# Kernel optimization log

Measured on AMD Instinct MI355X. Metric: run time of the kernel, lower is better.

Reference implementation:

```python
import jax, jax.numpy as jnp
import numpy as np

N = 100000   # nodes
E = 3200000  # edges (avg degree 32)
F_IN = 128   # nfeat
H = 128      # nhid
C = 40       # nclass
L = 3        # nlayers (GRU steps in GatedGraphConv)
BN_EPS = 1e-5


def _uniform(k, shape, scale):
    return jax.random.uniform(k, shape, jnp.float32, -scale, scale)


def setup_inputs() -> dict:
    key = jax.random.key(0)
    ks = jax.random.split(key, 12)
    h = jax.random.normal(ks[0], (N, F_IN), jnp.float32)
    edge_index = jax.random.randint(ks[1], (2, E), 0, N, dtype=jnp.int64)
    edge_weight = jax.random.uniform(ks[2], (E,), jnp.float32)
    s_h = 1.0 / np.sqrt(H)
    s_f = 1.0 / np.sqrt(F_IN)
    emb_W = _uniform(ks[3], (F_IN, H), s_f)
    emb_b = _uniform(ks[4], (H,), s_f)
    conv_weight = _uniform(ks[5], (L, H, H), s_h)      # PyG GatedGraphConv.weight
    gru_Wih = _uniform(ks[6], (3 * H, H), s_h)         # torch GRUCell weight_ih
    gru_Whh = _uniform(ks[7], (3 * H, H), s_h)
    gru_bih = _uniform(ks[8], (3 * H,), s_h)
    gru_bhh = _uniform(ks[9], (3 * H,), s_h)
    bn_gamma = jnp.ones((H,), jnp.float32)
    bn_beta = jnp.zeros((H,), jnp.float32)
    mlp_W = _uniform(ks[10], (H, C), s_h)
    mlp_b = _uniform(ks[11], (C,), s_h)
    return {"h": h, "edge_index": edge_index, "edge_weight": edge_weight,
            "emb_W": emb_W, "emb_b": emb_b, "conv_weight": conv_weight,
            "gru_Wih": gru_Wih, "gru_Whh": gru_Whh, "gru_bih": gru_bih,
            "gru_bhh": gru_bhh, "bn_gamma": bn_gamma, "bn_beta": bn_beta,
            "mlp_W": mlp_W, "mlp_b": mlp_b}


def reference(h, edge_index, edge_weight, emb_W, emb_b, conv_weight,
              gru_Wih, gru_Whh, gru_bih, gru_bhh, bn_gamma, bn_beta,
              mlp_W, mlp_b):
    src, dst = edge_index[0], edge_index[1]
    x = h @ emb_W + emb_b                      # [N, H] embedding_h
    h_in = x                                   # residual tap (before conv)
    for i in range(L):                         # GatedGraphConv GRU steps
        m = x @ conv_weight[i]                 # [N, H]
        msg = edge_weight[:, None] * m[src]    # [E, H] gather + weight
        agg = jax.ops.segment_sum(msg, dst, num_segments=N)  # scatter-add
        gi = agg @ gru_Wih.T + gru_bih         # [N, 3H]
        gh = x @ gru_Whh.T + gru_bhh
        i_r, i_z, i_n = jnp.split(gi, 3, axis=1)
        h_r, h_z, h_n = jnp.split(gh, 3, axis=1)
        r = jax.nn.sigmoid(i_r + h_r)
        z = jax.nn.sigmoid(i_z + h_z)
        n = jnp.tanh(i_n + r * h_n)
        x = (1.0 - z) * n + z * x              # GRUCell update
    mean = jnp.mean(x, axis=0)                 # BatchNorm1d (training stats)
    var = jnp.var(x, axis=0)
    x = (x - mean) / jnp.sqrt(var + BN_EPS) * bn_gamma + bn_beta
    x = h_in + x                               # residual; dropout p=0 is identity
    return x @ mlp_W + mlp_b                   # [N, C]
```

## Files before the change

### kernel.cpp

```cpp
#include <hip/hip_runtime.h>
#include <math.h>

#define N_NODES 100000
#define N_EDGES 3200000
#define HDIM 128

#define NB 196
#define BSH 9
#define BSLOT 18432

typedef __attribute__((ext_vector_type(8))) short bf16x8;
typedef __attribute__((ext_vector_type(4))) float f32x4;

__device__ __forceinline__ unsigned short f2bf(float f) {
  union { float f; unsigned u; } v; v.f = f;
  unsigned r = v.u + 0x7fffu + ((v.u >> 16) & 1u);
  return (unsigned short)(r >> 16);
}
__device__ __forceinline__ float bflo(unsigned p) {
  union { unsigned u; float f; } v; v.u = p << 16; return v.f;
}
__device__ __forceinline__ float bfhi(unsigned p) {
  union { unsigned u; float f; } v; v.u = p & 0xffff0000u; return v.f;
}
__device__ __forceinline__ float fsigmoid(float v) {
  return __builtin_amdgcn_rcpf(1.f + __expf(-v));
}
__device__ __forceinline__ float ftanh(float v) {
  return 1.f - 2.f * __builtin_amdgcn_rcpf(1.f + __expf(2.f * v));
}

__global__ __launch_bounds__(256) void zero_i32(int* __restrict__ p, int n) {
  int i = blockIdx.x * 256 + threadIdx.x;
  if (i < n) p[i] = 0;
}
__global__ __launch_bounds__(256) void zero_f32(float* __restrict__ p, int n) {
  int i = blockIdx.x * 256 + threadIdx.x;
  if (i < n) p[i] = 0.f;
}

__global__ __launch_bounds__(256) void repack_frag_b(
    const float* __restrict__ src, short* __restrict__ dst)
{
  int o = blockIdx.x * 256 + threadIdx.x;
  if (o >= 384 * 128) return;
  int j    = o & 7;
  int lane = (o >> 3) & 63;
  int ks   = (o >> 9) & 3;
  int t    = o >> 11;
  int m  = lane & 15;
  int g4 = lane >> 4;
  dst[o] = (short)f2bf(src[(t * 16 + m) * 128 + ks * 32 + g4 * 8 + j]);
}

template<bool BT>
__global__ __launch_bounds__(256) void gemm_k128(
    const float* __restrict__ A, const float* __restrict__ W,
    const float* __restrict__ bias, float* __restrict__ Y,
    unsigned* __restrict__ xpack, int M, int OUT)
{
  __shared__ alignas(16) float lds_a[32 * 68];
  __shared__ alignas(16) float lds_b[32 * 132];
  const int tid = threadIdx.x;
  const int tx = tid & 15;
  const int ty = tid >> 4;
  const int rowBase = blockIdx.x * 64;
  const int colBase = blockIdx.y * 128;

  float acc[4][8];
#pragma unroll
  for (int r = 0; r < 4; r++)
#pragma unroll
    for (int c = 0; c < 8; c++) acc[r][c] = 0.f;

  for (int k0 = 0; k0 < 128; k0 += 32) {
#pragma unroll
    for (int i = 0; i < 2; i++) {
      int idx = tid + i * 256;
      int r   = idx >> 3;
      int kk  = (idx & 7) << 2;
      int gr  = rowBase + r;
      float4 v = make_float4(0.f, 0.f, 0.f, 0.f);
      if (gr < M) v = *(const float4*)(A + (size_t)gr * HDIM + k0 + kk);
      lds_a[(kk + 0) * 68 + r] = v.x;
      lds_a[(kk + 1) * 68 + r] = v.y;
      lds_a[(kk + 2) * 68 + r] = v.z;
      lds_a[(kk + 3) * 68 + r] = v.w;
    }
    if (!BT) {
#pragma unroll
      for (int i = 0; i < 4; i++) {
        int idx = tid + i * 256;
        int kk  = idx >> 5;
        int j   = (idx & 31) << 2;
        int gj  = colBase + j;
        float4 v = make_float4(0.f, 0.f, 0.f, 0.f);
        if (gj < OUT) v = *(const float4*)(W + (size_t)(k0 + kk) * OUT + gj);
        *((float4*)&lds_b[kk * 132 + j]) = v;
      }
    } else {
#pragma unroll
      for (int i = 0; i < 4; i++) {
        int idx = tid + i * 256;
        int j   = idx >> 3;
        int k4  = (idx & 7) << 2;
        int gj  = colBase + j;
        float4 v = make_float4(0.f, 0.f, 0.f, 0.f);
        if (gj < OUT) v = *(const float4*)(W + (size_t)gj * HDIM + k0 + k4);
        lds_b[(k4 + 0) * 132 + j] = v.x;
        lds_b[(k4 + 1) * 132 + j] = v.y;
        lds_b[(k4 + 2) * 132 + j] = v.z;
        lds_b[(k4 + 3) * 132 + j] = v.w;
      }
    }
    __syncthreads();
#pragma unroll 8
    for (int kk = 0; kk < 32; kk++) {
      float4 a4 = *(const float4*)&lds_a[kk * 68 + ty * 4];
      float4 b0 = *(const float4*)&lds_b[kk * 132 + tx * 8];
      float4 b1 = *(const float4*)&lds_b[kk * 132 + tx * 8 + 4];
      float av[4] = {a4.x, a4.y, a4.z, a4.w};
      float bv[8] = {b0.x, b0.y, b0.z, b0.w, b1.x, b1.y, b1.z, b1.w};
#pragma unroll
      for (int r = 0; r < 4; r++)
#pragma unroll
        for (int c = 0; c < 8; c++)
          acc[r][c] = fmaf(av[r], bv[c], acc[r][c]);
    }
    __syncthreads();
  }

  int col = colBase + tx * 8;
  if (col >= OUT) return;
  float bv[8];
#pragma unroll
  for (int c = 0; c < 8; c++) bv[c] = bias ? bias[col + c] : 0.f;
#pragma unroll
  for (int r = 0; r < 4; r++) {
    int gr = rowBase + ty * 4 + r;
    if (gr >= M) continue;
    float* yp = Y + (size_t)gr * OUT + col;
    float4 o0 = make_float4(acc[r][0] + bv[0], acc[r][1] + bv[1],
                            acc[r][2] + bv[2], acc[r][3] + bv[3]);
    float4 o1 = make_float4(acc[r][4] + bv[4], acc[r][5] + bv[5],
                            acc[r][6] + bv[6], acc[r][7] + bv[7]);
    *(float4*)yp       = o0;
    *(float4*)(yp + 4) = o1;
    if (xpack) {
      uint4 p;
      p.x = (unsigned)f2bf(o0.x) | ((unsigned)f2bf(o0.y) << 16);
      p.y = (unsigned)f2bf(o0.z) | ((unsigned)f2bf(o0.w) << 16);
      p.z = (unsigned)f2bf(o1.x) | ((unsigned)f2bf(o1.y) << 16);
      p.w = (unsigned)f2bf(o1.z) | ((unsigned)f2bf(o1.w) << 16);
      *(uint4*)&xpack[(size_t)gr * 64 + (col >> 1)] = p;
    }
  }
}

__global__ __launch_bounds__(256) void csr_part1(
    const int* __restrict__ ei, const float* __restrict__ ew,
    int* __restrict__ bcnt,
    int2* __restrict__ tmp)
{
  __shared__ int hist[NB];
  __shared__ int gbase[NB];
  const int tid = threadIdx.x;
  for (int i = tid; i < NB; i += 256) hist[i] = 0;
  __syncthreads();
  const int e0 = blockIdx.x * 2048 + tid * 8;
  const bool act = (e0 < N_EDGES);
  int4 s0, s1, d0, d1; float4 w0, w1;
  int rb[8];
  if (act) {
    s0 = *(const int4*)(ei + e0);
    s1 = *(const int4*)(ei + e0 + 4);
    d0 = *(const int4*)(ei + N_EDGES + e0);
    d1 = *(const int4*)(ei + N_EDGES + e0 + 4);
    w0 = *(const float4*)(ew + e0);
    w1 = *(const float4*)(ew + e0 + 4);
    int dv[8] = {d0.x, d0.y, d0.z, d0.w, d1.x, d1.y, d1.z, d1.w};
#pragma unroll
    for (int j = 0; j < 8; j++) {
      int b = dv[j] >> BSH;
      int r = atomicAdd(&hist[b], 1);
      rb[j] = (r << 8) | b;
    }
  }
  __syncthreads();
  for (int i = tid; i < NB; i += 256) {
    int c = hist[i];
    gbase[i] = c ? atomicAdd(&bcnt[i * 16], c) : 0;
  }
  __syncthreads();
  if (act) {
    int sv[8] = {s0.x, s0.y, s0.z, s0.w, s1.x, s1.y, s1.z, s1.w};
    int dv[8] = {d0.x, d0.y, d0.z, d0.w, d1.x, d1.y, d1.z, d1.w};
    int wv[8] = {__float_as_int(w0.x), __float_as_int(w0.y),
                 __float_as_int(w0.z), __float_as_int(w0.w),
                 __float_as_int(w1.x), __float_as_int(w1.y),
                 __float_as_int(w1.z), __float_as_int(w1.w)};
#pragma unroll
    for (int j = 0; j < 8; j++) {
      int b  = rb[j] & 255;
      int of = gbase[b] + (rb[j] >> 8);
      if (of < BSLOT)
        tmp[b * BSLOT + of] =
            make_int2(sv[j] | ((dv[j] & 511) << 17), wv[j]);
    }
  }
}

__global__ void csr_scanb(const int* __restrict__ bcnt,
                          int* __restrict__ bstart, int* __restrict__ rowptr)
{
  __shared__ int l[256];
  int t = threadIdx.x;
  int v = (t < NB) ? min(bcnt[t * 16], BSLOT) : 0;
  l[t] = v;
  __syncthreads();
  for (int off = 1; off < 256; off <<= 1) {
    int u = (t >= off) ? l[t - off] : 0;
    __syncthreads();
    l[t] += u;
    __syncthreads();
  }
  if (t < NB) bstart[t] = l[t] - v;
  if (t == 255) rowptr[N_NODES] = l[255];
}

__global__ __launch_bounds__(256) void csr_part2(
    const int2* __restrict__ tmp, const int* __restrict__ bcnt,
    const int* __restrict__ bstart, int* __restrict__ rowptr,
    int2* __restrict__ epak)
{
  __shared__ int cnt[512];
  __shared__ int lofs[512];
  __shared__ int s2[256];
  const int b      = blockIdx.x;
  const int tid    = threadIdx.x;
  const int nbase  = b << BSH;
  const int nn     = min(512, N_NODES - nbase);
  const int ecount = min(bcnt[b * 16], BSLOT);
  const long tbase = (long)b * BSLOT;
  const int obase  = bstart[b];
  for (int i = tid; i < 512; i += 256) cnt[i] = 0;
  __syncthreads();
  for (int e = tid; e < ecount; e += 256) {
    int2 rec = tmp[tbase + e];
    atomicAdd(&cnt[(rec.x >> 17) & 511], 1);
  }
  __syncthreads();
  int c0 = cnt[2 * tid], c1 = cnt[2 * tid + 1];
  s2[tid] = c0 + c1;
  __syncthreads();
  int inc = s2[tid];
  for (int off = 1; off < 256; off <<= 1) {
    int u = (tid >= off) ? s2[tid - off] : 0;
    __syncthreads();
    s2[tid] += u;
    __syncthreads();
  }
  int ex = s2[tid] - inc;
  lofs[2 * tid]     = ex;
  lofs[2 * tid + 1] = ex + c0;
  __syncthreads();
  for (int i = tid; i < nn; i += 256) rowptr[nbase + i] = obase + lofs[i];
  for (int i = tid; i < 512; i += 256) cnt[i] = 0;
  __syncthreads();
  for (int e = tid; e < ecount; e += 256) {
    int2 rec = tmp[tbase + e];
    int ldst = (rec.x >> 17) & 511;
    int r = atomicAdd(&cnt[ldst], 1);
    epak[obase + lofs[ldst] + r] = make_int2((rec.x & 0x1FFFF) << 8, rec.y);
  }
}

__global__ __launch_bounds__(256) void agg_pull(
    const unsigned* __restrict__ xbp, const int* __restrict__ rowptr,
    const int2* __restrict__ epak, unsigned* __restrict__ zbp)
{
  const int node =
      __builtin_amdgcn_readfirstlane(blockIdx.x * 4 + (threadIdx.x >> 6));
  const int lane = threadIdx.x & 63;
  const unsigned lane4 = lane * 4;
  const char* xbc = (const char*)xbp;
  int e = rowptr[node];
  const int s1 = rowptr[node + 1];
  float v0 = 0.f, v1 = 0.f;
  if ((e & 1) && e < s1) {
    int2 ep = epak[e++];
    unsigned p = *(const unsigned*)(xbc + (unsigned)ep.x + lane4);
    float w = __int_as_float(ep.y);
    v0 = fmaf(w, bflo(p), v0); v1 = fmaf(w, bfhi(p), v1);
  }
  const int n16 = e + ((s1 - e) & ~15);
  for (; e < n16; e += 16) {
    int4 q[8];
#pragma unroll
    for (int j = 0; j < 8; j++) q[j] = *(const int4*)(epak + e + 2 * j);
    unsigned p[16];
#pragma unroll
    for (int j = 0; j < 8; j++) {
      p[2 * j]     = *(const unsigned*)(xbc + (unsigned)q[j].x + lane4);
      p[2 * j + 1] = *(const unsigned*)(xbc + (unsigned)q[j].z + lane4);
    }
#pragma unroll
    for (int j = 0; j < 8; j++) {
      float wa = __int_as_float(q[j].y), wb = __int_as_float(q[j].w);
      v0 = fmaf(wa, bflo(p[2 * j]), v0);
      v1 = fmaf(wa, bfhi(p[2 * j]), v1);
      v0 = fmaf(wb, bflo(p[2 * j + 1]), v0);
      v1 = fmaf(wb, bfhi(p[2 * j + 1]), v1);
    }
  }
  const int n4 = e + ((s1 - e) & ~3);
  for (; e < n4; e += 4) {
    int4 qa = *(const int4*)(epak + e);
    int4 qb = *(const int4*)(epak + e + 2);
    unsigned p0 = *(const unsigned*)(xbc + (unsigned)qa.x + lane4);
    unsigned p1 = *(const unsigned*)(xbc + (unsigned)qa.z + lane4);
    unsigned p2 = *(const unsigned*)(xbc + (unsigned)qb.x + lane4);
    unsigned p3 = *(const unsigned*)(xbc + (unsigned)qb.z + lane4);
    float w0 = __int_as_float(qa.y), w1 = __int_as_float(qa.w);
    float w2 = __int_as_float(qb.y), w3 = __int_as_float(qb.w);
    v0 = fmaf(w0, bflo(p0), v0); v1 = fmaf(w0, bfhi(p0), v1);
    v0 = fmaf(w1, bflo(p1), v0); v1 = fmaf(w1, bfhi(p1), v1);
    v0 = fmaf(w2, bflo(p2), v0); v1 = fmaf(w2, bfhi(p2), v1);
    v0 = fmaf(w3, bflo(p3), v0); v1 = fmaf(w3, bfhi(p3), v1);
  }
  for (; e < s1; e++) {
    int2 ep = epak[e];
    unsigned p = *(const unsigned*)(xbc + (unsigned)ep.x + lane4);
    float w = __int_as_float(ep.y);
    v0 = fmaf(w, bflo(p), v0); v1 = fmaf(w, bfhi(p), v1);
  }
  zbp[(size_t)node * 64 + lane] =
      (unsigned)f2bf(v0) | ((unsigned)f2bf(v1) << 16);
}

__global__ __launch_bounds__(256, 4) void gru_fused(
    const short* __restrict__ zb, short* __restrict__ xb,
    float* __restrict__ x,
    const short* __restrict__ Fb, const short* __restrict__ Wb,
    const float* __restrict__ bih, const float* __restrict__ bhh)
{
  const int wave = threadIdx.x >> 6, lane = threadIdx.x & 63;
  const int m  = lane & 15;
  const int g4 = lane >> 4;
  const int rowBase = blockIdx.x * 32;
  const int t0 = wave * 2;

  f32x4 aR[2][2], aZ[2][2], aN[2][2], aH[2][2];
#pragma unroll
  for (int rt = 0; rt < 2; rt++)
#pragma unroll
    for (int ti = 0; ti < 2; ti++) {
      aR[rt][ti] = (f32x4){0.f, 0.f, 0.f, 0.f};
      aZ[rt][ti] = (f32x4){0.f, 0.f, 0.f, 0.f};
      aN[rt][ti] = (f32x4){0.f, 0.f, 0.f, 0.f};
      aH[rt][ti] = (f32x4){0.f, 0.f, 0.f, 0.f};
    }

  size_t arowc[2];
#pragma unroll
  for (int rt = 0; rt < 2; rt++)
    arowc[rt] = (size_t)(rowBase + rt * 16 + m) * 128 + g4 * 8;

#pragma unroll
  for (int ks = 0; ks < 4; ks++) {
    bf16x8 a[2];
#pragma unroll
    for (int rt = 0; rt < 2; rt++)
      a[rt] = *(const bf16x8*)(zb + arowc[rt] + ks * 32);
    const int bo = ks * 512 + lane * 8;
#pragma unroll
    for (int ti = 0; ti < 2; ti++) {
      const short* bp = Fb + (t0 + ti) * 2048 + bo;
      bf16x8 br = *(const bf16x8*)(bp);
      bf16x8 bz = *(const bf16x8*)(bp + 16384);
      bf16x8 bn = *(const bf16x8*)(bp + 32768);
#pragma unroll
      for (int rt = 0; rt < 2; rt++) {
        aR[rt][ti] = __builtin_amdgcn_mfma_f32_16x16x32_bf16(a[rt], br, aR[rt][ti], 0, 0, 0);
        aZ[rt][ti] = __builtin_amdgcn_mfma_f32_16x16x32_bf16(a[rt], bz, aZ[rt][ti], 0, 0, 0);
        aN[rt][ti] = __builtin_amdgcn_mfma_f32_16x16x32_bf16(a[rt], bn, aN[rt][ti], 0, 0, 0);
      }
    }
  }
#pragma unroll
  for (int ks = 0; ks < 4; ks++) {
    bf16x8 a[2];
#pragma unroll
    for (int rt = 0; rt < 2; rt++)
      a[rt] = *(const bf16x8*)(xb + arowc[rt] + ks * 32);
    const int bo = ks * 512 + lane * 8;
#pragma unroll
    for (int ti = 0; ti < 2; ti++) {
      const short* bp = Wb + (t0 + ti) * 2048 + bo;
      bf16x8 br = *(const bf16x8*)(bp);
      bf16x8 bz = *(const bf16x8*)(bp + 16384);
      bf16x8 bn = *(const bf16x8*)(bp + 32768);
#pragma unroll
      for (int rt = 0; rt < 2; rt++) {
        aR[rt][ti] = __builtin_amdgcn_mfma_f32_16x16x32_bf16(a[rt], br, aR[rt][ti], 0, 0, 0);
        aZ[rt][ti] = __builtin_amdgcn_mfma_f32_16x16x32_bf16(a[rt], bz, aZ[rt][ti], 0, 0, 0);
        aH[rt][ti] = __builtin_amdgcn_mfma_f32_16x16x32_bf16(a[rt], bn, aH[rt][ti], 0, 0, 0);
      }
    }
  }

  float xo[2][2][4];
  size_t xoff[2][2];
#pragma unroll
  for (int ti = 0; ti < 2; ti++)
#pragma unroll
    for (int rt = 0; rt < 2; rt++) {
      size_t o = (size_t)(rowBase + rt * 16 + g4 * 4) * 128 + (t0 + ti) * 16 + m;
      xoff[ti][rt] = o;
#pragma unroll
      for (int r = 0; r < 4; r++) xo[ti][rt][r] = x[o + (size_t)r * 128];
    }
#pragma unroll
  for (int ti = 0; ti < 2; ti++) {
    int col = (t0 + ti) * 16 + m;
    float b_r = bih[col] + bhh[col];
    float b_z = bih[128 + col] + bhh[128 + col];
    float b_i = bih[256 + col];
    float b_h = bhh[256 + col];
#pragma unroll
    for (int rt = 0; rt < 2; rt++) {
#pragma unroll
      for (int r = 0; r < 4; r++) {
        float rg = fsigmoid(aR[rt][ti][r] + b_r);
        float zg = fsigmoid(aZ[rt][ti][r] + b_z);
        float ng = ftanh(aN[rt][ti][r] + b_i + rg * (aH[rt][ti][r] + b_h));
        float xn = (1.f - zg) * ng + zg * xo[ti][rt][r];
        size_t o = xoff[ti][rt] + (size_t)r * 128;
        x[o] = xn;
        xb[o] = (short)f2bf(xn);
      }
    }
  }
}

__global__ __launch_bounds__(256) void bn_stats(
    const float* __restrict__ x, float* __restrict__ sums)
{
  __shared__ float ls[256], lq[256];
  int tid  = threadIdx.x;
  int col  = tid & 127, half = tid >> 7;
  int r0   = blockIdx.x * 128;
  int rend = min(N_NODES, r0 + 128);
  float s = 0.f, q = 0.f;
  for (int r = r0 + half; r < rend; r += 2) {
    float v = x[(size_t)r * HDIM + col];
    s += v; q += v * v;
  }
  ls[tid] = s; lq[tid] = q;
  __syncthreads();
  if (tid < 128) {
    atomicAdd(&sums[col],       ls[tid] + ls[tid + 128]);
    atomicAdd(&sums[128 + col], lq[tid] + lq[tid + 128]);
  }
}

__global__ void bn_finalize(float* __restrict__ sums,
                            const float* __restrict__ gamma,
                            const float* __restrict__ beta)
{
  int j = threadIdx.x;
  float mean = sums[j] / (float)N_NODES;
  float var  = sums[128 + j] / (float)N_NODES - mean * mean;
  float inv  = rsqrtf(var + 1e-5f);
  sums[256 + j] = gamma[j] * inv;
  sums[384 + j] = beta[j] - mean * gamma[j] * inv;
}

__global__ __launch_bounds__(256) void head_fused(
    const float* __restrict__ x, const float* __restrict__ h,
    const float* __restrict__ sums,
    const float* __restrict__ mlpW,
    const float* __restrict__ e2,
    const float* __restrict__ c2,
    float* __restrict__ out)
{
  __shared__ alignas(16) float lds_b[2][128][44];
  __shared__ alignas(16) float lds_a[32 * 260];
  const int tid = threadIdx.x;
  const int tx = tid & 7;
  const int ty = tid >> 3;
  const int rowBase = blockIdx.x * 256;

  for (int i = tid; i < 128 * 40; i += 256) {
    int kk = i / 40, j = i - kk * 40;
    lds_b[0][kk][j] = mlpW[i];
    lds_b[1][kk][j] = e2[i];
  }

  float acc[8][5];
#pragma unroll
  for (int r = 0; r < 8; r++)
#pragma unroll
    for (int c = 0; c < 5; c++) acc[r][c] = 0.f;

  for (int src = 0; src < 2; src++) {
    const float* A = src ? h : x;
    for (int k0 = 0; k0 < 128; k0 += 32) {
      __syncthreads();
#pragma unroll
      for (int i = 0; i < 8; i++) {
        int idx = tid + i * 256;
        int r   = idx >> 3;
        int kk  = (idx & 7) << 2;
        int gr  = rowBase + r;
        float4 v = make_float4(0.f, 0.f, 0.f, 0.f);
        if (gr < N_NODES) v = *(const float4*)(A + (size_t)gr * HDIM + k0 + kk);
        if (src == 0) {
          float4 sc = *(const float4*)(sums + 256 + k0 + kk);
          float4 sh = *(const float4*)(sums + 384 + k0 + kk);
          v.x = fmaf(v.x, sc.x, sh.x);
          v.y = fmaf(v.y, sc.y, sh.y);
          v.z = fmaf(v.z, sc.z, sh.z);
          v.w = fmaf(v.w, sc.w, sh.w);
        }
        lds_a[(kk + 0) * 260 + r] = v.x;
        lds_a[(kk + 1) * 260 + r] = v.y;
        lds_a[(kk + 2) * 260 + r] = v.z;
        lds_a[(kk + 3) * 260 + r] = v.w;
      }
      __syncthreads();
#pragma unroll 4
      for (int kk = 0; kk < 32; kk++) {
        float4 b4 = *(const float4*)&lds_b[src][k0 + kk][tx * 4];
        float  b1 = lds_b[src][k0 + kk][32 + tx];
        float4 a0 = *(const float4*)&lds_a[kk * 260 + ty * 8];
        float4 a1 = *(const float4*)&lds_a[kk * 260 + ty * 8 + 4];
        float av[8] = {a0.x, a0.y, a0.z, a0.w, a1.x, a1.y, a1.z, a1.w};
#pragma unroll
        for (int r = 0; r < 8; r++) {
          acc[r][0] = fmaf(av[r], b4.x, acc[r][0]);
          acc[r][1] = fmaf(av[r], b4.y, acc[r][1]);
          acc[r][2] = fmaf(av[r], b4.z, acc[r][2]);
          acc[r][3] = fmaf(av[r], b4.w, acc[r][3]);
          acc[r][4] = fmaf(av[r], b1,   acc[r][4]);
        }
      }
    }
  }

  const int c0 = tx * 4, c4 = 32 + tx;
  float bv0 = c2[c0], bv1 = c2[c0 + 1], bv2 = c2[c0 + 2], bv3 = c2[c0 + 3];
  float bv4 = c2[c4];
#pragma unroll
  for (int r = 0; r < 8; r++) {
    int gr = rowBase + ty * 8 + r;
    if (gr >= N_NODES) continue;
    float* yp = out + (size_t)gr * 40;
    float4 o = make_float4(acc[r][0] + bv0, acc[r][1] + bv1,
                           acc[r][2] + bv2, acc[r][3] + bv3);
    *(float4*)(yp + c0) = o;
    yp[c4] = acc[r][4] + bv4;
  }
}

__global__ __launch_bounds__(256) void prep_e2(
    const float* __restrict__ embW,
    const float* __restrict__ embB,
    const float* __restrict__ mlpW,
    const float* __restrict__ mlpB,
    float* __restrict__ e2, float* __restrict__ c2)
{
  int idx = blockIdx.x * 256 + threadIdx.x;
  if (idx < 5120) {
    int f = idx / 40, j = idx - f * 40;
    const float* er = embW + f * 128;
    float s = 0.f;
    for (int k = 0; k < 128; k++)
      s = fmaf(er[k], mlpW[k * 40 + j], s);
    e2[idx] = s;
  } else if (idx < 5160) {
    int j = idx - 5120;
    float s = mlpB[j];
    for (int k = 0; k < 128; k++)
      s = fmaf(embB[k], mlpW[k * 40 + j], s);
    c2[j] = s;
  }
}

extern "C" void kernel_launch(void* const* d_in, const int* in_sizes, int n_in,
                              void* d_out, int out_size, void* d_ws, size_t ws_size,
                              hipStream_t stream)
{
  const float* h     = (const float*)d_in[0];
  const int*   ei    = (const int*)d_in[1];
  const float* ew    = (const float*)d_in[2];
  const float* embW  = (const float*)d_in[3];
  const float* embB  = (const float*)d_in[4];
  const float* convW = (const float*)d_in[5];
  const float* Wih   = (const float*)d_in[6];
  const float* Whh   = (const float*)d_in[7];
  const float* bih   = (const float*)d_in[8];
  const float* bhh   = (const float*)d_in[9];
  const float* gamma = (const float*)d_in[10];
  const float* beta  = (const float*)d_in[11];
  const float* mlpW  = (const float*)d_in[12];
  const float* mlpB  = (const float*)d_in[13];
  float* out = (float*)d_out;

  float* ws = (float*)d_ws;
  const size_t NH = (size_t)N_NODES * HDIM;
  float*    x      = ws;
  unsigned* xbp    = (unsigned*)(ws + NH);
  unsigned* zbp    = xbp + NH / 2;
  int2*     epak   = (int2*)(zbp + NH / 2);
  int*      rowptr = (int*)(epak + N_EDGES);
  int*      bcnt   = rowptr + N_NODES + 4;
  int*      bstart = bcnt + NB * 16;
  float*    Ffold  = (float*)(bstart + 256);
  short*    Fbp    = (short*)(Ffold + 3 * 384 * 128);
  short*    Wbp    = Fbp + 3 * 384 * 128;
  float*    sums   = (float*)(Wbp + 384 * 128);
  float*    e2     = sums + 512;
  float*    c2     = e2 + 5120;
  int2*     tmp    = (int2*)xbp;

  dim3 blk(256);
  const int MB = (N_NODES + 63) / 64;
  const int GB = N_NODES / 32;
  const int HB = (N_NODES + 255) / 256;
  const int RB = (384 * 128 + 255) / 256;
  const int P1B = (N_EDGES + 2047) / 2048;

  prep_e2<<<21, blk, 0, stream>>>(embW, embB, mlpW, mlpB, e2, c2);
  for (int l = 0; l < 3; l++)
    gemm_k128<true><<<dim3(6, 1), blk, 0, stream>>>(
        Wih, convW + (size_t)l * HDIM * HDIM, nullptr,
        Ffold + (size_t)l * 384 * HDIM, nullptr, 384, 128);
  for (int l = 0; l < 3; l++)
    repack_frag_b<<<RB, blk, 0, stream>>>(
        Ffold + (size_t)l * 384 * HDIM, Fbp + (size_t)l * 384 * HDIM);
  repack_frag_b<<<RB, blk, 0, stream>>>(Whh, Wbp);

  zero_i32<<<(NB * 16 + 255) / 256, blk, 0, stream>>>(bcnt, NB * 16);
  csr_part1<<<P1B, blk, 0, stream>>>(ei, ew, bcnt, tmp);
  csr_scanb<<<1, 256, 0, stream>>>(bcnt, bstart, rowptr);
  csr_part2<<<NB, blk, 0, stream>>>(tmp, bcnt, bstart, rowptr, epak);

  gemm_k128<false><<<dim3(MB, 1), blk, 0, stream>>>(h, embW, embB, x, xbp,
                                                    N_NODES, 128);

  for (int l = 0; l < 3; l++) {
    agg_pull<<<N_NODES / 4, blk, 0, stream>>>(xbp, rowptr, epak, zbp);
    gru_fused<<<GB, blk, 0, stream>>>(
        (const short*)zbp, (short*)xbp, x,
        Fbp + (size_t)l * 384 * HDIM, Wbp, bih, bhh);
  }

  zero_f32<<<2, blk, 0, stream>>>(sums, 512);
  bn_stats<<<(N_NODES + 127) / 128, blk, 0, stream>>>(x, sums);
  bn_finalize<<<1, 128, 0, stream>>>(sums, gamma, beta);
  head_fused<<<HB, blk, 0, stream>>>(x, h, sums, mlpW, e2, c2, out);
}
```

Measured before the change: 950.5 us.

## Split aggregation into column slices with edge-parallel lane groups per wave

The pull aggregation kernel now splits the 128 feature columns into 4 slices, one per blockIdx.x, and gives each wave 4 lane groups of 16 lanes. Each group handles a different edge, and the partial sums are combined with cross-lane shuffles. Edge records are read with nontemporal loads. The aim is more independent gathers in flight and a grid ordered so that column slices of the source rows stay in cache. In exchange, the edge list and rowptr are read four times, the deep unrolled batching is gone, and there is extra shuffle-reduction work.

New measurement: 1.572 ms. 1.65x slower.

```diff
diff --git a/kernel.cpp b/kernel.cpp
--- a/kernel.cpp
+++ b/kernel.cpp
@@ -279,63 +279,39 @@
     const unsigned* __restrict__ xbp, const int* __restrict__ rowptr,
     const int2* __restrict__ epak, unsigned* __restrict__ zbp)
 {
-  const int node =
-      __builtin_amdgcn_readfirstlane(blockIdx.x * 4 + (threadIdx.x >> 6));
+  const int s    = blockIdx.x;
+  const int node = blockIdx.y * 4 + (threadIdx.x >> 6);
   const int lane = threadIdx.x & 63;
-  const unsigned lane4 = lane * 4;
+  const int g    = lane >> 4;
+  const unsigned coff = s * 64 + (lane & 15) * 4;
   const char* xbc = (const char*)xbp;
+  const long long* epq = (const long long*)epak;
   int e = rowptr[node];
   const int s1 = rowptr[node + 1];
   float v0 = 0.f, v1 = 0.f;
-  if ((e & 1) && e < s1) {
-    int2 ep = epak[e++];
-    unsigned p = *(const unsigned*)(xbc + (unsigned)ep.x + lane4);
-    float w = __int_as_float(ep.y);
-    v0 = fmaf(w, bflo(p), v0); v1 = fmaf(w, bfhi(p), v1);
-  }
-  const int n16 = e + ((s1 - e) & ~15);
-  for (; e < n16; e += 16) {
-    int4 q[8];
-#pragma unroll
-    for (int j = 0; j < 8; j++) q[j] = *(const int4*)(epak + e + 2 * j);
-    unsigned p[16];
-#pragma unroll
-    for (int j = 0; j < 8; j++) {
-      p[2 * j]     = *(const unsigned*)(xbc + (unsigned)q[j].x + lane4);
-      p[2 * j + 1] = *(const unsigned*)(xbc + (unsigned)q[j].z + lane4);
-    }
-#pragma unroll
-    for (int j = 0; j < 8; j++) {
-      float wa = __int_as_float(q[j].y), wb = __int_as_float(q[j].w);
-      v0 = fmaf(wa, bflo(p[2 * j]), v0);
-      v1 = fmaf(wa, bfhi(p[2 * j]), v1);
-      v0 = fmaf(wb, bflo(p[2 * j + 1]), v0);
-      v1 = fmaf(wb, bfhi(p[2 * j + 1]), v1);
-    }
-  }
-  const int n4 = e + ((s1 - e) & ~3);
-  for (; e < n4; e += 4) {
-    int4 qa = *(const int4*)(epak + e);
-    int4 qb = *(const int4*)(epak + e + 2);
-    unsigned p0 = *(const unsigned*)(xbc + (unsigned)qa.x + lane4);
-    unsigned p1 = *(const unsigned*)(xbc + (unsigned)qa.z + lane4);
-    unsigned p2 = *(const unsigned*)(xbc + (unsigned)qb.x + lane4);
-    unsigned p3 = *(const unsigned*)(xbc + (unsigned)qb.z + lane4);
-    float w0 = __int_as_float(qa.y), w1 = __int_as_float(qa.w);
-    float w2 = __int_as_float(qb.y), w3 = __int_as_float(qb.w);
-    v0 = fmaf(w0, bflo(p0), v0); v1 = fmaf(w0, bfhi(p0), v1);
-    v0 = fmaf(w1, bflo(p1), v0); v1 = fmaf(w1, bfhi(p1), v1);
-    v0 = fmaf(w2, bflo(p2), v0); v1 = fmaf(w2, bfhi(p2), v1);
-    v0 = fmaf(w3, bflo(p3), v0); v1 = fmaf(w3, bfhi(p3), v1);
-  }
-  for (; e < s1; e++) {
-    int2 ep = epak[e];
-    unsigned p = *(const unsigned*)(xbc + (unsigned)ep.x + lane4);
-    float w = __int_as_float(ep.y);
-    v0 = fmaf(w, bflo(p), v0); v1 = fmaf(w, bfhi(p), v1);
-  }
-  zbp[(size_t)node * 64 + lane] =
-      (unsigned)f2bf(v0) | ((unsigned)f2bf(v1) << 16);
+  for (; e + 8 <= s1; e += 8) {
+    long long qa = __builtin_nontemporal_load(epq + e + g);
+    long long qb = __builtin_nontemporal_load(epq + e + g + 4);
+    unsigned pa = *(const unsigned*)(xbc + (unsigned)(int)qa + coff);
+    unsigned pb = *(const unsigned*)(xbc + (unsigned)(int)qb + coff);
+    float wa = __int_as_float((int)(qa >> 32));
+    float wb = __int_as_float((int)(qb >> 32));
+    v0 = fmaf(wa, bflo(pa), v0); v1 = fmaf(wa, bfhi(pa), v1);
+    v0 = fmaf(wb, bflo(pb), v0); v1 = fmaf(wb, bfhi(pb), v1);
+  }
+  for (; e < s1; e += 4) {
+    if (e + g < s1) {
+      long long qa = __builtin_nontemporal_load(epq + e + g);
+      unsigned pa = *(const unsigned*)(xbc + (unsigned)(int)qa + coff);
+      float wa = __int_as_float((int)(qa >> 32));
+      v0 = fmaf(wa, bflo(pa), v0); v1 = fmaf(wa, bfhi(pa), v1);
+    }
+  }
+  v0 += __shfl_xor(v0, 16, 64); v0 += __shfl_xor(v0, 32, 64);
+  v1 += __shfl_xor(v1, 16, 64); v1 += __shfl_xor(v1, 32, 64);
+  if (g == 0)
+    zbp[(size_t)node * 64 + s * 16 + (lane & 15)] =
+        (unsigned)f2bf(v0) | ((unsigned)f2bf(v1) << 16);
 }
 
 __global__ __launch_bounds__(256, 4) void gru_fused(
@@ -650,7 +626,7 @@
                                                     N_NODES, 128);
 
   for (int l = 0; l < 3; l++) {
-    agg_pull<<<N_NODES / 4, blk, 0, stream>>>(xbp, rowptr, epak, zbp);
+    agg_pull<<<dim3(4, N_NODES / 4), blk, 0, stream>>>(xbp, rowptr, epak, zbp);
     gru_fused<<<GB, blk, 0, stream>>>(
         (const short*)zbp, (short*)xbp, x,
         Fbp + (size_t)l * 384 * HDIM, Wbp, bih, bhh);
```
